# Kernel tuning notes

Measured on AMD Instinct MI355X. Metric: run time of the kernel, lower is better.

## Reference

```python
import jax, jax.numpy as jnp
import numpy as np

B, S, D, H, DFF = 2, 2048, 1024, 16, 4096
DK = D // H
EPS = 1e-6


def setup_inputs() -> dict:
    key = jax.random.key(0)
    ks = jax.random.split(key, 16)
    sd = 0.02
    inp = {
        "x": jax.random.normal(ks[0], (B, S, D), jnp.float32),
        "mask": jnp.zeros((1, 1, S, S), jnp.float32),
        "wq": jax.random.normal(ks[1], (D, D), jnp.float32) * sd,
        "bq": jnp.zeros((D,), jnp.float32),
        "wk": jax.random.normal(ks[2], (D, D), jnp.float32) * sd,
        "bk": jnp.zeros((D,), jnp.float32),
        "wv": jax.random.normal(ks[3], (D, D), jnp.float32) * sd,
        "bv": jnp.zeros((D,), jnp.float32),
        "wo": jax.random.normal(ks[4], (D, D), jnp.float32) * sd,
        "bo": jnp.zeros((D,), jnp.float32),
        "w1": jax.random.normal(ks[5], (DFF, D), jnp.float32) * sd,
        "b1": jnp.zeros((DFF,), jnp.float32),
        "w2": jax.random.normal(ks[6], (D, DFF), jnp.float32) * sd,
        "b2": jnp.zeros((D,), jnp.float32),
        "alpha": jnp.ones((1,), jnp.float32),
        "gamma": jnp.zeros((1,), jnp.float32),
    }
    return inp


def _layer_norm(x, alpha, gamma):
    mean = jnp.mean(x, axis=-1, keepdims=True)
    var = jnp.mean((x - mean) ** 2, axis=-1, keepdims=True)
    return alpha * (x - mean) / jnp.sqrt(var + EPS) + gamma


def reference(x, mask, wq, bq, wk, bk, wv, bv, wo, bo, w1, b1, w2, b2, alpha, gamma):
    # --- multi-head attention (hand-rolled, full NxN scores) ---
    q = (x @ wq.T + bq).reshape(B, S, H, DK).transpose(0, 2, 1, 3)  # [B,H,S,DK]
    k = (x @ wk.T + bk).reshape(B, S, H, DK).transpose(0, 2, 1, 3)
    v = (x @ wv.T + bv).reshape(B, S, H, DK).transpose(0, 2, 1, 3)
    scores = jnp.einsum('bhqd,bhkd->bhqk', q, k) / np.sqrt(DK)  # [B,H,S,S]
    scores = scores + mask
    attn = jax.nn.softmax(scores, axis=-1)
    ctx = jnp.einsum('bhqk,bhkd->bhqd', attn, v)  # [B,H,S,DK]
    ctx = ctx.transpose(0, 2, 1, 3).reshape(B, S, D)
    attn_out = ctx @ wo.T + bo
    # residual + LayerNorm (dropout is identity in eval)
    out1 = _layer_norm(x + attn_out, alpha, gamma)
    # --- position-wise feed-forward ---
    ffn = jax.nn.relu(out1 @ w1.T + b1) @ w2.T + b2
    out2 = _layer_norm(out1 + ffn, alpha, gamma)
    return out2
```

## Files before the change

### kernel.cpp

```cpp
#include <hip/hip_runtime.h>


typedef float  f32x4   __attribute__((ext_vector_type(4)));
typedef float  f32x16  __attribute__((ext_vector_type(16)));
typedef __bf16 bf16x8  __attribute__((ext_vector_type(8)));
typedef __bf16 bf16x4  __attribute__((ext_vector_type(4)));

#define DEVI static __device__ __forceinline__

DEVI f32x4 mfma16(bf16x8 a, bf16x8 b, f32x4 c) {
    return __builtin_amdgcn_mfma_f32_16x16x32_bf16(a, b, c, 0, 0, 0);
}
DEVI f32x16 mfma32(bf16x8 a, bf16x8 b, f32x16 c) {
    return __builtin_amdgcn_mfma_f32_32x32x16_bf16(a, b, c, 0, 0, 0);
}

DEVI void gll16(const void* g, void* l) {
    __builtin_amdgcn_global_load_lds(
        (__attribute__((address_space(1))) void*)g,
        (__attribute__((address_space(3))) void*)l, 16, 0, 0);
}

DEVI __bf16 f2bf(float f) { return (__bf16)f; }

DEVI unsigned cvtpk_bf16(float a, float b) {
    unsigned d;
    asm("v_cvt_pk_bf16_f32 %0, %1, %2" : "=v"(d) : "v"(a), "v"(b));
    return d;
}
DEVI void permswap(unsigned& a, unsigned& b) {
    asm("v_permlane32_swap_b32 %0, %1" : "+v"(a), "+v"(b));
}
DEVI void permswapf(float& a, float& b) {
    asm("v_permlane32_swap_b32 %0, %1" : "+v"(a), "+v"(b));
}

__global__ void init_flag_kernel(int* f) { *f = 0; }

__global__ void mask_scan_kernel(const float* __restrict__ m, int* __restrict__ flag) {
    size_t i = (size_t)blockIdx.x * 256 + threadIdx.x;
    const float4* p = (const float4*)m;
    float4 a = p[i * 2], b = p[i * 2 + 1];
    bool nz = a.x != 0.f || a.y != 0.f || a.z != 0.f || a.w != 0.f ||
              b.x != 0.f || b.y != 0.f || b.z != 0.f || b.w != 0.f;
    if (__ballot(nz)) { if ((threadIdx.x & 63) == 0) atomicOr(flag, 1); }
}

__global__ void cast_bf16_kernel(const float* __restrict__ in, __bf16* __restrict__ out, int n8) {
    int i = blockIdx.x * 256 + threadIdx.x;
    if (i >= n8) return;
    const float4* p = (const float4*)in + (size_t)i * 2;
    float4 a = p[0], b = p[1];
    bf16x8 o = { (__bf16)a.x, (__bf16)a.y, (__bf16)a.z, (__bf16)a.w,
                 (__bf16)b.x, (__bf16)b.y, (__bf16)b.z, (__bf16)b.w };
    *(bf16x8*)(out + (size_t)i * 8) = o;
}

__global__ __launch_bounds__(256) void cast_weights_kernel(
    const float* __restrict__ wq, const float* __restrict__ wk,
    const float* __restrict__ wv, const float* __restrict__ wo,
    const float* __restrict__ w1, const float* __restrict__ w2,
    __bf16* __restrict__ wqb, __bf16* __restrict__ wkb,
    __bf16* __restrict__ wvb, __bf16* __restrict__ wob,
    __bf16* __restrict__ w1b, __bf16* __restrict__ w2b) {
    int i = blockIdx.x * 256 + threadIdx.x;
    const float* src; __bf16* dst; int off;
    if      (i <  131072) { src = wq; dst = wqb; off = i; }
    else if (i <  262144) { src = wk; dst = wkb; off = i -  131072; }
    else if (i <  393216) { src = wv; dst = wvb; off = i -  262144; }
    else if (i <  524288) { src = wo; dst = wob; off = i -  393216; }
    else if (i < 1048576) { src = w1; dst = w1b; off = i -  524288; }
    else                  { src = w2; dst = w2b; off = i - 1048576; }
    const float4* p = (const float4*)src + (size_t)off * 2;
    float4 a = p[0], b = p[1];
    bf16x8 o = { (__bf16)a.x, (__bf16)a.y, (__bf16)a.z, (__bf16)a.w,
                 (__bf16)b.x, (__bf16)b.y, (__bf16)b.z, (__bf16)b.w };
    *(bf16x8*)(dst + (size_t)off * 8) = o;
}

__global__ __launch_bounds__(256) void add_ln_kernel(
    const float* __restrict__ X, const float* __restrict__ Y,
    const float* __restrict__ alphap, const float* __restrict__ gammap,
    float* __restrict__ outF, __bf16* __restrict__ outB) {
    const int tid = threadIdx.x, lane = tid & 63, wid = tid >> 6;
    const size_t base = (size_t)blockIdx.x * 1024 + tid * 4;
    float4 xv = *(const float4*)&X[base];
    float4 yv = *(const float4*)&Y[base];
    float vx = xv.x + yv.x, vy = xv.y + yv.y, vz = xv.z + yv.z, vw = xv.w + yv.w;
    float s = vx + vy + vz + vw;
    #pragma unroll
    for (int o = 32; o; o >>= 1) s += __shfl_xor(s, o);
    __shared__ float red[4];
    if (lane == 0) red[wid] = s;
    __syncthreads();
    float mean = (red[0] + red[1] + red[2] + red[3]) * (1.0f / 1024.0f);
    float dx = vx - mean, dy = vy - mean, dz = vz - mean, dw = vw - mean;
    float s2 = dx * dx + dy * dy + dz * dz + dw * dw;
    #pragma unroll
    for (int o = 32; o; o >>= 1) s2 += __shfl_xor(s2, o);
    __syncthreads();
    if (lane == 0) red[wid] = s2;
    __syncthreads();
    float var = (red[0] + red[1] + red[2] + red[3]) * (1.0f / 1024.0f);
    float rstd = rsqrtf(var + 1e-6f);
    float a = alphap[0], g = gammap[0];
    float4 o4 = { a * dx * rstd + g, a * dy * rstd + g, a * dz * rstd + g, a * dw * rstd + g };
    *(float4*)&outF[base] = o4;
    if (outB) {
        bf16x4 ob = { f2bf(o4.x), f2bf(o4.y), f2bf(o4.z), f2bf(o4.w) };
        *(bf16x4*)&outB[base] = ob;
    }
}

template <int N, int K, int BN, int MODE>
__global__ __launch_bounds__(256, 3) void gemm_bt_kernel(
    const __bf16* __restrict__ A, const __bf16* __restrict__ W,
    const float* __restrict__ bias, void* __restrict__ outp) {
    constexpr int WN = BN / 2;
    constexpr int NI = WN / 16;
    __shared__ __bf16 lsA[128 * 64];
    __shared__ __bf16 lsB[BN * 64];
    const int tid = threadIdx.x, wid = tid >> 6, lane = tid & 63;
    const int wr = wid >> 1, wc = wid & 1, l15 = lane & 15, hi = lane >> 4;
    const int m0 = blockIdx.y * 128, n0 = blockIdx.x * BN;
    f32x4 acc[4][NI] = {};
    for (int kt = 0; kt < K / 64; ++kt) {
        #pragma unroll
        for (int i = 0; i < 4; ++i) {
            int row = wid * 32 + i * 8 + (lane >> 3);
            gll16(A + (size_t)(m0 + row) * K + kt * 64 + ((lane & 7) ^ (row & 7)) * 8,
                  &lsA[(wid * 32 + i * 8) * 64]);
        }
        #pragma unroll
        for (int i = 0; i < BN / 32; ++i) {
            int row = wid * (BN / 4) + i * 8 + (lane >> 3);
            gll16(W + (size_t)(n0 + row) * K + kt * 64 + ((lane & 7) ^ (row & 7)) * 8,
                  &lsB[(wid * (BN / 4) + i * 8) * 64]);
        }
        __syncthreads();
        #pragma unroll
        for (int s = 0; s < 2; ++s) {
            bf16x8 af[4], bfv[NI];
            #pragma unroll
            for (int mi = 0; mi < 4; ++mi) {
                int row = wr * 64 + mi * 16 + l15;
                af[mi] = *(const bf16x8*)&lsA[row * 64 + (((s * 4 + hi) ^ (row & 7)) * 8)];
            }
            #pragma unroll
            for (int ni = 0; ni < NI; ++ni) {
                int row = wc * WN + ni * 16 + l15;
                bfv[ni] = *(const bf16x8*)&lsB[row * 64 + (((s * 4 + hi) ^ (row & 7)) * 8)];
            }
            #pragma unroll
            for (int mi = 0; mi < 4; ++mi)
                #pragma unroll
                for (int ni = 0; ni < NI; ++ni)
                    acc[mi][ni] = mfma16(af[mi], bfv[ni], acc[mi][ni]);
        }
        __syncthreads();
    }
    #pragma unroll
    for (int ni = 0; ni < NI; ++ni) {
        int col = n0 + wc * WN + ni * 16 + l15;
        float bv = bias[col];
        #pragma unroll
        for (int mi = 0; mi < 4; ++mi) {
            int rowb = m0 + wr * 64 + mi * 16 + hi * 4;
            #pragma unroll
            for (int r = 0; r < 4; ++r) {
                float v = acc[mi][ni][r] + bv;
                if (MODE == 0) {
                    ((float*)outp)[(size_t)(rowb + r) * N + col] = v;
                } else {
                    v = fmaxf(v, 0.f);
                    ((__bf16*)outp)[(size_t)(rowb + r) * N + col] = f2bf(v);
                }
            }
        }
    }
}

__global__ __launch_bounds__(256, 3) void gemm_qkv_kernel(
    const __bf16* __restrict__ A,
    const __bf16* __restrict__ wq, const __bf16* __restrict__ wk, const __bf16* __restrict__ wv,
    const float* __restrict__ bq, const float* __restrict__ bk, const float* __restrict__ bv,
    __bf16* __restrict__ q, __bf16* __restrict__ k, __bf16* __restrict__ vt) {
    constexpr int K = 1024;
    const int z = blockIdx.z;
    const __bf16* W = (z == 0) ? wq : (z == 1) ? wk : wv;
    const float* bias = (z == 0) ? bq : (z == 1) ? bk : bv;
    __shared__ __bf16 lsA[128 * 64];
    __shared__ __bf16 lsB[128 * 64];
    const int tid = threadIdx.x, wid = tid >> 6, lane = tid & 63;
    const int wr = wid >> 1, wc = wid & 1, l15 = lane & 15, hi = lane >> 4;
    const int m0 = blockIdx.y * 128, n0 = blockIdx.x * 128;
    f32x4 acc[4][4] = {};
    for (int kt = 0; kt < K / 64; ++kt) {
        #pragma unroll
        for (int i = 0; i < 4; ++i) {
            int row = wid * 32 + i * 8 + (lane >> 3);
            gll16(A + (size_t)(m0 + row) * K + kt * 64 + ((lane & 7) ^ (row & 7)) * 8,
                  &lsA[(wid * 32 + i * 8) * 64]);
            gll16(W + (size_t)(n0 + row) * K + kt * 64 + ((lane & 7) ^ (row & 7)) * 8,
                  &lsB[(wid * 32 + i * 8) * 64]);
        }
        __syncthreads();
        #pragma unroll
        for (int s = 0; s < 2; ++s) {
            bf16x8 af[4], bfv[4];
            #pragma unroll
            for (int mi = 0; mi < 4; ++mi) {
                int row = wr * 64 + mi * 16 + l15;
                af[mi] = *(const bf16x8*)&lsA[row * 64 + (((s * 4 + hi) ^ (row & 7)) * 8)];
            }
            #pragma unroll
            for (int ni = 0; ni < 4; ++ni) {
                int row = wc * 64 + ni * 16 + l15;
                bfv[ni] = *(const bf16x8*)&lsB[row * 64 + (((s * 4 + hi) ^ (row & 7)) * 8)];
            }
            #pragma unroll
            for (int mi = 0; mi < 4; ++mi)
                #pragma unroll
                for (int ni = 0; ni < 4; ++ni)
                    acc[mi][ni] = mfma16(af[mi], bfv[ni], acc[mi][ni]);
        }
        __syncthreads();
    }
    const float scale = (z == 0) ? 0.125f * 1.4426950408889634f : 1.0f;
    #pragma unroll
    for (int ni = 0; ni < 4; ++ni) {
        int col = n0 + wc * 64 + ni * 16 + l15;
        int h = col >> 6, dk = col & 63;
        float bvv = bias[col];
        #pragma unroll
        for (int mi = 0; mi < 4; ++mi) {
            int rowb = m0 + wr * 64 + mi * 16 + hi * 4;
            int b_ = rowb >> 11, sb = rowb & 2047;
            if (z < 2) {
                __bf16* dst = (z == 0) ? q : k;
                #pragma unroll
                for (int r = 0; r < 4; ++r)
                    dst[((size_t)(b_ * 16 + h) * 2048 + sb + r) * 64 + dk] =
                        f2bf((acc[mi][ni][r] + bvv) * scale);
            } else {
                bf16x4 o = { f2bf(acc[mi][ni][0] + bvv), f2bf(acc[mi][ni][1] + bvv),
                             f2bf(acc[mi][ni][2] + bvv), f2bf(acc[mi][ni][3] + bvv) };
                *(bf16x4*)&vt[((size_t)(b_ * 16 + h) * 64 + dk) * 2048 + sb] = o;
            }
        }
    }
}

__global__ __launch_bounds__(256, 2) void flash_attn_kernel(
    const __bf16* __restrict__ Q, const __bf16* __restrict__ Kx,
    const __bf16* __restrict__ VT, const float* __restrict__ mask,
    const int* __restrict__ mflag, __bf16* __restrict__ ctx) {
    __shared__ __bf16 Kl[2][64 * 64];
    __shared__ __bf16 Vl[2][64 * 64];
    const int lane = threadIdx.x & 63, wid = threadIdx.x >> 6;
    const int l31 = lane & 31, h = lane >> 5;
    const int id = blockIdx.x;
    const int xcd = id & 7, rest = id >> 3;
    const int qt = rest & 15;
    const int bh = (rest >> 4) * 8 + xcd;
    const int q0 = qt * 128 + wid * 32;

    bf16x8 qf[4];
    const size_t qrow = (size_t)bh * 2048 + q0 + l31;
    #pragma unroll
    for (int st = 0; st < 4; ++st)
        qf[st] = *(const bf16x8*)&Q[qrow * 64 + st * 16 + h * 8];

    const __bf16* kbase = Kx + (size_t)bh * 2048 * 64;
    const __bf16* vbase = VT + (size_t)bh * 64 * 2048;

    f32x16 c0 = {}, c1 = {};
    f32x16 lv = {};
    const bool useMask = (*mflag != 0);

    const int r0 = wid * 16;
    const int rA = r0 + (lane >> 3);
    const int rB = rA + 8;
    const int cA = (lane & 7) ^ (rA & 7);
    const int cB = (lane & 7) ^ (rB & 7);

    auto stage = [&](int b, int t) {
        gll16(kbase + (size_t)(t * 64 + rA) * 64 + cA * 8, &Kl[b][r0 * 64]);
        gll16(kbase + (size_t)(t * 64 + rB) * 64 + cB * 8, &Kl[b][(r0 + 8) * 64]);
        gll16(vbase + (size_t)rA * 2048 + t * 64 + cA * 8, &Vl[b][r0 * 64]);
        gll16(vbase + (size_t)rB * 2048 + t * 64 + cB * 8, &Vl[b][(r0 + 8) * 64]);
    };

    stage(0, 0);
    __syncthreads();
    int cur = 0;

    for (int t = 0; t < 32; ++t) {
        const int tn = (t + 1 < 32) ? t + 1 : t;
        stage(cur ^ 1, tn);
        #pragma unroll
        for (int s = 0; s < 2; ++s) {
            const int krow = s * 32 + l31;
            f32x16 sc = {};
            __builtin_amdgcn_s_setprio(1);
            #pragma unroll
            for (int st = 0; st < 4; ++st) {
                bf16x8 kf = *(const bf16x8*)&Kl[cur][krow * 64 + (((st * 2 + h) ^ (krow & 7)) * 8)];
                sc = mfma32(kf, qf[st], sc);
            }
            __builtin_amdgcn_s_setprio(0);
            if (useMask) {
                #pragma unroll
                for (int r = 0; r < 16; ++r) {
                    int kv = t * 64 + s * 32 + (r & 3) + 8 * (r >> 2) + 4 * h;
                    sc[r] += mask[(size_t)(q0 + l31) * 2048 + kv] * 1.4426950408889634f;
                }
            }
            #pragma unroll
            for (int r = 0; r < 16; ++r) sc[r] = exp2f(sc[r] - 40.0f);
            lv += sc;
            unsigned w0 = cvtpk_bf16(sc[0], sc[1]),   w2 = cvtpk_bf16(sc[4], sc[5]);
            unsigned w1 = cvtpk_bf16(sc[2], sc[3]),   w3 = cvtpk_bf16(sc[6], sc[7]);
            permswap(w0, w2); permswap(w1, w3);
            unsigned w4 = cvtpk_bf16(sc[8], sc[9]),   w6 = cvtpk_bf16(sc[12], sc[13]);
            unsigned w5 = cvtpk_bf16(sc[10], sc[11]), w7 = cvtpk_bf16(sc[14], sc[15]);
            permswap(w4, w6); permswap(w5, w7);
            uint4 u0 = { w0, w1, w2, w3 }, u1 = { w4, w5, w6, w7 };
            bf16x8 pb0, pb1;
            __builtin_memcpy(&pb0, &u0, 16);
            __builtin_memcpy(&pb1, &u1, 16);
            const int vr0 = l31, vr1 = 32 + l31;
            bf16x8 v00 = *(const bf16x8*)&Vl[cur][vr0 * 64 + (((s * 4 + 0 + h) ^ (vr0 & 7)) * 8)];
            bf16x8 v01 = *(const bf16x8*)&Vl[cur][vr0 * 64 + (((s * 4 + 2 + h) ^ (vr0 & 7)) * 8)];
            bf16x8 v10 = *(const bf16x8*)&Vl[cur][vr1 * 64 + (((s * 4 + 0 + h) ^ (vr1 & 7)) * 8)];
            bf16x8 v11 = *(const bf16x8*)&Vl[cur][vr1 * 64 + (((s * 4 + 2 + h) ^ (vr1 & 7)) * 8)];
            __builtin_amdgcn_s_setprio(1);
            c0 = mfma32(v00, pb0, c0);
            c0 = mfma32(v01, pb1, c0);
            c1 = mfma32(v10, pb0, c1);
            c1 = mfma32(v11, pb1, c1);
            __builtin_amdgcn_s_setprio(0);
        }
        __syncthreads();
        cur ^= 1;
    }

    float y8[8], y4[4];
    #pragma unroll
    for (int r = 0; r < 8; ++r) y8[r] = lv[2 * r] + lv[2 * r + 1];
    #pragma unroll
    for (int r = 0; r < 4; ++r) y4[r] = y8[2 * r] + y8[2 * r + 1];
    float ls = (y4[0] + y4[1]) + (y4[2] + y4[3]);
    float la = ls, lb = ls;
    permswapf(la, lb);
    const float rinv = 1.0f / (la + lb);

    const int b_ = bh >> 4, h_ = bh & 15;
    const size_t obase = ((size_t)b_ * 2048 + q0 + l31) * 1024 + (size_t)h_ * 64;
    #pragma unroll
    for (int g = 0; g < 4; ++g) {
        bf16x4 o0 = { f2bf(c0[4 * g + 0] * rinv), f2bf(c0[4 * g + 1] * rinv),
                      f2bf(c0[4 * g + 2] * rinv), f2bf(c0[4 * g + 3] * rinv) };
        *(bf16x4*)&ctx[obase + g * 8 + h * 4] = o0;
        bf16x4 o1 = { f2bf(c1[4 * g + 0] * rinv), f2bf(c1[4 * g + 1] * rinv),
                      f2bf(c1[4 * g + 2] * rinv), f2bf(c1[4 * g + 3] * rinv) };
        *(bf16x4*)&ctx[obase + 32 + g * 8 + h * 4] = o1;
    }
}

extern "C" void kernel_launch(void* const* d_in, const int* in_sizes, int n_in,
                              void* d_out, int out_size, void* d_ws, size_t ws_size,
                              hipStream_t stream) {
    const float* x     = (const float*)d_in[0];
    const float* mask  = (const float*)d_in[1];
    const float* wq    = (const float*)d_in[2];
    const float* bq    = (const float*)d_in[3];
    const float* wk    = (const float*)d_in[4];
    const float* bk    = (const float*)d_in[5];
    const float* wv    = (const float*)d_in[6];
    const float* bv    = (const float*)d_in[7];
    const float* wo    = (const float*)d_in[8];
    const float* bo    = (const float*)d_in[9];
    const float* w1    = (const float*)d_in[10];
    const float* b1    = (const float*)d_in[11];
    const float* w2    = (const float*)d_in[12];
    const float* b2    = (const float*)d_in[13];
    const float* alpha = (const float*)d_in[14];
    const float* gamma = (const float*)d_in[15];

    char* ws = (char*)d_ws;
    const size_t MB = 1u << 20;
    __bf16* xb    = (__bf16*)(ws + 0 * MB);
    __bf16* qb    = (__bf16*)(ws + 8 * MB);
    __bf16* kb    = (__bf16*)(ws + 16 * MB);
    __bf16* vtb   = (__bf16*)(ws + 24 * MB);
    __bf16* ctxb  = (__bf16*)(ws + 32 * MB);
    __bf16* wqb   = (__bf16*)(ws + 40 * MB);
    __bf16* wkb   = (__bf16*)(ws + 42 * MB);
    __bf16* wvb   = (__bf16*)(ws + 44 * MB);
    __bf16* wob   = (__bf16*)(ws + 46 * MB);
    __bf16* w1b   = (__bf16*)(ws + 48 * MB);
    __bf16* w2b   = (__bf16*)(ws + 56 * MB);
    float*  attn  = (float*)(ws + 64 * MB);
    float*  out1  = (float*)(ws + 80 * MB);
    __bf16* out1b = (__bf16*)(ws + 96 * MB);
    __bf16* hid   = (__bf16*)(ws + 104 * MB);
    int*    mflag = (int*)(ws + 136 * MB);
    if (ws_size < 136 * MB + 64) return;

    init_flag_kernel<<<1, 1, 0, stream>>>(mflag);
    mask_scan_kernel<<<2048, 256, 0, stream>>>(mask, mflag);

    cast_bf16_kernel<<<2048, 256, 0, stream>>>(x, xb, 524288);
    cast_weights_kernel<<<6144, 256, 0, stream>>>(wq, wk, wv, wo, w1, w2,
                                                  wqb, wkb, wvb, wob, w1b, w2b);

    gemm_qkv_kernel<<<dim3(8, 32, 3), 256, 0, stream>>>(xb, wqb, wkb, wvb, bq, bk, bv,
                                                        qb, kb, vtb);
    flash_attn_kernel<<<dim3(512), 256, 0, stream>>>(qb, kb, vtb, mask, mflag, ctxb);
    gemm_bt_kernel<1024, 1024, 64, 0><<<dim3(16, 32), 256, 0, stream>>>(ctxb, wob, bo, attn);
    add_ln_kernel<<<4096, 256, 0, stream>>>(x, attn, alpha, gamma, out1, out1b);
    gemm_bt_kernel<4096, 1024, 128, 1><<<dim3(32, 32), 256, 0, stream>>>(out1b, w1b, b1, hid);
    gemm_bt_kernel<1024, 4096, 64, 0><<<dim3(16, 32), 256, 0, stream>>>(hid, w2b, b2, attn);
    add_ln_kernel<<<4096, 256, 0, stream>>>(out1, attn, alpha, gamma, (float*)d_out, nullptr);
}
```

Before: 264.7 us.

## Add triple-buffered 256x128 tile GEMM for FFN up-projection

Replaces the FFN W1 GEMM with a new kernel that uses 512 threads, 256x128 output tiles, and a three-stage LDS ring filled by global_load_lds with XOR swizzle. Loads for tile t+2 are issued while tile t is computed, with explicit vmcnt waits and s_setprio around the MFMA section. Block indices are remapped for L2 locality. The kernel uses a large LDS footprint (about 144KB), which limits it to one block per CU and depends on latency hiding within the block.

```diff
diff --git a/kernel.cpp b/kernel.cpp
--- a/kernel.cpp
+++ b/kernel.cpp
@@ -175,6 +175,91 @@
                     v = fmaxf(v, 0.f);
                     ((__bf16*)outp)[(size_t)(rowb + r) * N + col] = f2bf(v);
                 }
+            }
+        }
+    }
+}
+
+template <int N, int K>
+__global__ __launch_bounds__(512, 1) void gemm_pipe_kernel(
+    const __bf16* __restrict__ A, const __bf16* __restrict__ W,
+    const float* __restrict__ bias, __bf16* __restrict__ outp) {
+    constexpr int NT = K / 64;
+    __shared__ __bf16 lsA[3][256 * 64];
+    __shared__ __bf16 lsB[3][128 * 64];
+    const int tid = threadIdx.x, wid = tid >> 6, lane = tid & 63;
+    const int wr = wid >> 1, wc = wid & 1, l15 = lane & 15, hi = lane >> 4;
+    const int bid = blockIdx.x;
+    const int tile = (bid & 7) * 64 + (bid >> 3);
+    const int m0 = (tile >> 5) * 256, n0 = (tile & 31) * 128;
+
+    f32x4 acc[4][4] = {};
+
+    const int rl = wid * 8 + (lane >> 3);
+    const int c8 = lane & 7;
+
+    auto stageT = [&](int slot, int kt) {
+        #pragma unroll
+        for (int j = 0; j < 4; ++j) {
+            int r = j * 64 + rl;
+            gll16(A + (size_t)(m0 + r) * K + kt * 64 + (c8 ^ (r & 7)) * 8,
+                  &lsA[slot][(j * 64 + wid * 8) * 64]);
+        }
+        #pragma unroll
+        for (int j = 0; j < 2; ++j) {
+            int r = j * 64 + rl;
+            gll16(W + (size_t)(n0 + r) * K + kt * 64 + (c8 ^ (r & 7)) * 8,
+                  &lsB[slot][(j * 64 + wid * 8) * 64]);
+        }
+    };
+
+    stageT(0, 0);
+    stageT(1, 1);
+    asm volatile("s_waitcnt vmcnt(6)\ns_barrier" ::: "memory");
+
+    for (int t = 0; t < NT; ++t) {
+        if (t + 2 < NT) stageT((t + 2) % 3, t + 2);
+        const __bf16* As = &lsA[t % 3][0];
+        const __bf16* Bs = &lsB[t % 3][0];
+        __builtin_amdgcn_s_setprio(1);
+        #pragma unroll
+        for (int s = 0; s < 2; ++s) {
+            bf16x8 af[4], bfv[4];
+            #pragma unroll
+            for (int mi = 0; mi < 4; ++mi) {
+                int row = wr * 64 + mi * 16 + l15;
+                af[mi] = *(const bf16x8*)&As[row * 64 + (((s * 4 + hi) ^ (row & 7)) * 8)];
+            }
+            #pragma unroll
+            for (int ni = 0; ni < 4; ++ni) {
+                int row = wc * 64 + ni * 16 + l15;
+                bfv[ni] = *(const bf16x8*)&Bs[row * 64 + (((s * 4 + hi) ^ (row & 7)) * 8)];
+            }
+            #pragma unroll
+            for (int mi = 0; mi < 4; ++mi)
+                #pragma unroll
+                for (int ni = 0; ni < 4; ++ni)
+                    acc[mi][ni] = mfma16(af[mi], bfv[ni], acc[mi][ni]);
+        }
+        __builtin_amdgcn_s_setprio(0);
+        if (t < NT - 2) {
+            asm volatile("s_waitcnt vmcnt(6)\ns_barrier" ::: "memory");
+        } else if (t == NT - 2) {
+            asm volatile("s_waitcnt vmcnt(0)\ns_barrier" ::: "memory");
+        }
+    }
+
+    #pragma unroll
+    for (int ni = 0; ni < 4; ++ni) {
+        int col = n0 + wc * 64 + ni * 16 + l15;
+        float bv = bias[col];
+        #pragma unroll
+        for (int mi = 0; mi < 4; ++mi) {
+            int rowb = m0 + wr * 64 + mi * 16 + hi * 4;
+            #pragma unroll
+            for (int r = 0; r < 4; ++r) {
+                float v = fmaxf(acc[mi][ni][r] + bv, 0.f);
+                outp[(size_t)(rowb + r) * N + col] = f2bf(v);
             }
         }
     }
@@ -420,7 +505,7 @@
     flash_attn_kernel<<<dim3(512), 256, 0, stream>>>(qb, kb, vtb, mask, mflag, ctxb);
     gemm_bt_kernel<1024, 1024, 64, 0><<<dim3(16, 32), 256, 0, stream>>>(ctxb, wob, bo, attn);
     add_ln_kernel<<<4096, 256, 0, stream>>>(x, attn, alpha, gamma, out1, out1b);
-    gemm_bt_kernel<4096, 1024, 128, 1><<<dim3(32, 32), 256, 0, stream>>>(out1b, w1b, b1, hid);
+    gemm_pipe_kernel<4096, 1024><<<dim3(512), 512, 0, stream>>>(out1b, w1b, b1, hid);
     gemm_bt_kernel<1024, 4096, 64, 0><<<dim3(16, 32), 256, 0, stream>>>(hid, w2b, b2, attn);
     add_ln_kernel<<<4096, 256, 0, stream>>>(out1, attn, alpha, gamma, (float*)d_out, nullptr);
 }
```

Result: slower. 273.3 us (+3.2%).
